# Optimization experiments

Hardware: AMD Instinct MI355X
Metric: run time of the kernel (lower is better)

Reference implementation:

```python
import jax, jax.numpy as jnp
import numpy as np

C = 256          # conv_channels
C1 = C // 2      # 128
C2 = C // 4      # 64
G = 1            # relation_glimpse


def setup_inputs() -> dict:
    key = jax.random.key(0)
    ks = jax.random.split(key, 20)
    bs, Nr, in_dim, q_dim = 4, 256, 2052, 1024
    d_in = in_dim + 4  # pos (first 4 coords) re-appended
    s = 0.02
    inp = {
        "Q": jax.random.normal(ks[0], (bs, q_dim), jnp.float32),
        "X": jax.random.normal(ks[1], (bs, Nr, in_dim), jnp.float32),
        "Wv": jax.random.normal(ks[2], (d_in, C), jnp.float32) * s,
        "bv": jnp.zeros((C,), jnp.float32),
        "Wq": jax.random.normal(ks[3], (q_dim, C), jnp.float32) * s,
        "bq": jnp.zeros((C,), jnp.float32),
        # branch 0 (r_conv01/02/03): 1x1 convs == per-position dense
        "W01": jax.random.normal(ks[4], (C, C1), jnp.float32) * s,
        "b01": jnp.zeros((C1,), jnp.float32),
        "W02": jax.random.normal(ks[5], (C1, C2), jnp.float32) * s,
        "b02": jnp.zeros((C2,), jnp.float32),
        "W03": jax.random.normal(ks[6], (C2, G), jnp.float32) * s,
        "b03": jnp.zeros((G,), jnp.float32),
        # branch 1 (r_conv1/2/3): dilation on 1x1 kernels is a no-op
        "W1": jax.random.normal(ks[7], (C, C1), jnp.float32) * s,
        "b1": jnp.zeros((C1,), jnp.float32),
        "W2": jax.random.normal(ks[8], (C1, C2), jnp.float32) * s,
        "b2": jnp.zeros((C2,), jnp.float32),
        "W3": jax.random.normal(ks[9], (C2, G), jnp.float32) * s,
        "b3": jnp.zeros((G,), jnp.float32),
    }
    return inp


def _mlp3(P, Wa, ba, Wb, bb, Wc, bc):
    # P: [bs, Nr, Nr, C]; three 1x1-conv layers, ReLU after each (incl. last).
    h = jax.nn.relu(jnp.einsum("bijc,ck->bijk", P, Wa) + ba)
    h = jax.nn.relu(jnp.einsum("bijc,ck->bijk", h, Wb) + bb)
    h = jax.nn.relu(jnp.einsum("bijc,ck->bijk", h, Wc) + bc)
    return h[..., 0]  # [bs, Nr, Nr] (relation_glimpse == 1)


def _attn_map(h):
    # symmetrize, then softmax over all Nr*Nr positions
    s = h + jnp.swapaxes(h, 1, 2)
    bs, Nr, _ = s.shape
    return jax.nn.softmax(s.reshape(bs, Nr * Nr), axis=-1).reshape(bs, Nr, Nr)


def reference(Q, X, Wv, bv, Wq, bq, W01, b01, W02, b02, W03, b03,
              W1, b1, W2, b2, W3, b3):
    X_ = X
    # append pos (first 4 coords) -> [bs, Nr, in_dim+4]
    Xcat = jnp.concatenate([X, X[:, :, :4]], axis=2)
    Xp = jnp.einsum("bnd,dc->bnc", Xcat, Wv) + bv
    Qp = Q @ Wq + bq
    Xp = Xp + Qp[:, None, :]                       # [bs, Nr, C]
    P = Xp[:, None, :, :] * Xp[:, :, None, :]      # [bs, Nr, Nr, C] pairwise product
    m0 = _attn_map(_mlp3(P, W01, b01, W02, b02, W03, b03))
    m1 = _attn_map(_mlp3(P, W1, b1, W2, b2, W3, b3))
    # weighted aggregation with original features; /(2*glimpse), then sum over Nr
    rel = jnp.einsum("bij,bjd->bid", m0 + m1, X_) / (2.0 * G)
    return rel.sum(axis=1)  # [bs, in_dim]
```

## Files before the change

kernel.cpp:

```cpp
#include <hip/hip_runtime.h>
#include <hip/hip_bf16.h>

typedef __attribute__((ext_vector_type(8)))  short short8;
typedef __attribute__((ext_vector_type(4)))  float f32x4;
typedef __attribute__((ext_vector_type(16))) float f32x16;

#define NR 256
#define CC 256

__device__ __forceinline__ unsigned short f2bf(float x) {
    union { float f; unsigned int u; } v; v.f = x;
    unsigned int r = v.u + 0x7FFFu + ((v.u >> 16) & 1u);
    return (unsigned short)(r >> 16);
}

__device__ __forceinline__ unsigned int pk2bf(float a, float b) {
    __hip_bfloat162 h = __float22bfloat162_rn(make_float2(a, b));
    union { __hip_bfloat162 h; unsigned int u; } cv; cv.h = h;
    return cv.u;
}

__global__ __launch_bounds__(256) void setup_kernel(
    const float* __restrict__ Q, const float* __restrict__ Wq, float* __restrict__ Qpp,
    const float* __restrict__ Wv, unsigned short* __restrict__ wvp,
    const float* __restrict__ W01, const float* __restrict__ W1,
    const float* __restrict__ W02, const float* __restrict__ W2,
    unsigned short* __restrict__ wpa, unsigned short* __restrict__ wpb)
{
    __shared__ float tile[32][260];
    __shared__ float qs[256];
    const int bx = blockIdx.x;
    const int tid = threadIdx.x;

    if (bx < 16) {
        int ksl = bx & 3, b = bx >> 2;
        qs[tid] = Q[b * 1024 + ksl * 256 + tid];
        __syncthreads();
        float acc = 0.f;
        #pragma unroll 4
        for (int d = 0; d < 256; ++d) acc += qs[d] * Wq[(size_t)(ksl * 256 + d) * 256 + tid];
        Qpp[(ksl * 4 + b) * 256 + tid] = acc;
    } else if (bx < 81) {
        int ks = bx - 16;
        for (int idx = tid; idx < 32 * 256; idx += 256) {
            int cr = idx >> 8, n = idx & 255;
            int c = ks * 32 + cr;
            tile[cr][n] = (c < 2056) ? Wv[(size_t)c * 256 + n] : 0.f;
        }
        __syncthreads();
        #pragma unroll
        for (int q = 0; q < 4; ++q) {
            int t2 = tid * 4 + q;
            int nt = t2 >> 6, l = t2 & 63;
            int gg = l >> 4, jj = l & 15;
            short8 s;
            #pragma unroll
            for (int e = 0; e < 8; ++e)
                s[e] = (short)f2bf(tile[gg * 8 + e][nt * 16 + jj]);
            *(short8*)&wvp[((size_t)(ks * 16 + nt) * 64 + l) * 8] = s;
        }
    } else {
        int t = (bx - 81) * 256 + tid;
        if (t < 65536) {
            int e = t & 7, l = (t >> 3) & 63, ks = (t >> 9) & 15, nt = (t >> 13) & 3, br = (t >> 15) & 1;
            int cc = ks * 16 + (l >> 5) * 8 + e;
            int n = nt * 32 + (l & 31);
            const float* W = br ? W1 : W01;
            wpa[t] = f2bf(W[cc * 128 + n]);
        } else {
            int t2 = t - 65536;
            int e = t2 & 7, l = (t2 >> 3) & 63, ks = (t2 >> 9) & 7, nt = (t2 >> 12) & 1, br = (t2 >> 13) & 1;
            int cc = ks * 16 + (l >> 5) * 8 + e;
            int n = nt * 32 + (l & 31);
            const float* W = br ? W2 : W02;
            wpb[t2] = f2bf(W[cc * 64 + n]);
        }
    }
}

__global__ __launch_bounds__(512) void xp_kernel(
    const float* __restrict__ X, const unsigned short* __restrict__ wvp,
    const float* __restrict__ bv, const float* __restrict__ bq,
    const float* __restrict__ Qpp, float* __restrict__ Xp)
{
    __shared__ f32x4 red[8][2][65];
    const int tid = threadIdx.x;
    const int w = tid >> 6;
    const int lane = tid & 63;
    const int g = lane >> 4, j16 = lane & 15;
    const int mt = blockIdx.x;
    const int bn = blockIdx.y;
    const int b  = blockIdx.z;

    const int i0 = mt * 16;
    const int n0 = bn * 32;
    const float* xrow = X + ((size_t)(b * NR) + (i0 + j16)) * 2052;

    f32x4 acc[2] = {};

    for (int ks = w; ks < 64; ks += 8) {
        const int c0 = ks * 32 + g * 8;
        float4 xa = *(const float4*)(xrow + c0);
        float4 xb = *(const float4*)(xrow + c0 + 4);
        union { short8 s; unsigned int u[4]; } af;
        af.u[0] = pk2bf(xa.x, xa.y);
        af.u[1] = pk2bf(xa.z, xa.w);
        af.u[2] = pk2bf(xb.x, xb.y);
        af.u[3] = pk2bf(xb.z, xb.w);
        #pragma unroll
        for (int nt = 0; nt < 2; ++nt) {
            short8 bf = ((const short8*)wvp)[(size_t)(ks * 16 + bn * 2 + nt) * 64 + lane];
            acc[nt] = __builtin_amdgcn_mfma_f32_16x16x32_bf16(af.s, bf, acc[nt], 0, 0, 0);
        }
    }
    if (w == 0) {
        float xv[8];
        #pragma unroll
        for (int e = 0; e < 8; ++e) {
            int q = g * 8 + e;
            int csrc = (q < 4) ? (2048 + q) : (q - 4);
            xv[e] = xrow[csrc];
        }
        union { short8 s; unsigned int u[4]; } af;
        af.u[0] = pk2bf(xv[0], xv[1]);
        af.u[1] = pk2bf(xv[2], xv[3]);
        af.u[2] = pk2bf(xv[4], xv[5]);
        af.u[3] = pk2bf(xv[6], xv[7]);
        #pragma unroll
        for (int nt = 0; nt < 2; ++nt) {
            short8 bf = ((const short8*)wvp)[(size_t)(64 * 16 + bn * 2 + nt) * 64 + lane];
            acc[nt] = __builtin_amdgcn_mfma_f32_16x16x32_bf16(af.s, bf, acc[nt], 0, 0, 0);
        }
    }
    #pragma unroll
    for (int nt = 0; nt < 2; ++nt) red[w][nt][lane] = acc[nt];
    __syncthreads();

    {
        int nt  = tid >> 8;
        int rem = tid & 255;
        int l   = rem & 63;
        int reg = (rem >> 6) & 3;
        float r = 0.f;
        #pragma unroll
        for (int ww = 0; ww < 8; ++ww) r += red[ww][nt][l][reg];
        int gg = l >> 4, jj = l & 15;
        int n = n0 + nt * 16 + jj;
        float base = bv[n] + bq[n] + Qpp[b * 256 + n] + Qpp[(4 + b) * 256 + n]
                   + Qpp[(8 + b) * 256 + n] + Qpp[(12 + b) * 256 + n];
        int row = i0 + gg * 4 + reg;
        Xp[((b * NR) + row) * CC + n] = r + base;
    }
}

__global__ __launch_bounds__(256, 2) void pairs_kernel(
    const float* __restrict__ Xp,
    const unsigned short* __restrict__ wpa,
    const unsigned short* __restrict__ wpb,
    const float* __restrict__ b01, const float* __restrict__ b02,
    const float* __restrict__ b03,
    const float* __restrict__ b1,  const float* __restrict__ b2,
    const float* __restrict__ b3,
    const float* __restrict__ W03, const float* __restrict__ W3,
    float* __restrict__ colpart, float* __restrict__ rowpart)
{
    __shared__ __align__(16) unsigned short lds_wa[16384];
    __shared__ __align__(16) float lds_si[1024];
    __shared__ __align__(16) float lds_bias1[128];
    __shared__ __align__(16) float lds_bias2[64];
    __shared__ __align__(16) float lds_w3[64];
    __shared__ float lds_c[4][33];

    const int tid = threadIdx.x;
    const int wave = tid >> 6;
    const int lane = tid & 63;
    const int hi = lane >> 5;
    const int j32 = lane & 31;

    int bx = blockIdx.x;
    int b = bx / 576;
    int r = bx - b * 576;
    int br = r / 288;
    int u = r - br * 288;
    int k = 0, off = 0;
    while (u >= off + 8 * (8 - k)) { off += 8 * (8 - k); ++k; }
    int rel = u - off, wdt = 8 - k;
    int it = k * 8 + rel / wdt;
    int jt = k + rel % wdt;

    const int i0 = it * 4;
    const int i = i0 + wave;
    const int j0 = jt * 32;
    const int blk = br * 4 + b;

    {
        int c4 = lane * 4;
        *(float4*)&lds_si[wave * 256 + c4] =
            *(const float4*)&Xp[((b * NR) + i) * CC + c4];
    }

    {
        const uint4* gsrc = (const uint4*)(wpa + (size_t)br * 32768);
        uint4* sdst = (uint4*)lds_wa;
        #pragma unroll
        for (int kk = 0; kk < 8; ++kk) sdst[kk * 256 + tid] = gsrc[kk * 256 + tid];
    }
    if (tid < 128) lds_bias1[tid] = br ? b1[tid] : b01[tid];
    else if (tid < 192) lds_bias2[tid - 128] = br ? b2[tid - 128] : b02[tid - 128];
    else lds_w3[tid - 192] = br ? W3[tid - 192] : W03[tid - 192];
    const float b3v = br ? b3[0] : b03[0];

    const float* xr = Xp + ((size_t)(b * NR) + (j0 + j32)) * CC;
    const float* si = lds_si + wave * 256;
    short8 bfr[16];
    #pragma unroll
    for (int ks = 0; ks < 16; ++ks) {
        const int c0 = ks * 16 + hi * 8;
        float4 xa = *(const float4*)(xr + c0);
        float4 xb = *(const float4*)(xr + c0 + 4);
        float4 sa = *(const float4*)(si + c0);
        float4 sb = *(const float4*)(si + c0 + 4);
        union { short8 s; unsigned int u[4]; } f;
        f.u[0] = pk2bf(xa.x * sa.x, xa.y * sa.y);
        f.u[1] = pk2bf(xa.z * sa.z, xa.w * sa.w);
        f.u[2] = pk2bf(xb.x * sb.x, xb.y * sb.y);
        f.u[3] = pk2bf(xb.z * sb.z, xb.w * sb.w);
        bfr[ks] = f.s;
    }

    __syncthreads();

    const short8* gwa = (const short8*)wpa + (size_t)br * 4096;
    const short8* wb  = (const short8*)wpb + (size_t)br * 1024;

    f32x16 acc2[2];
    #pragma unroll
    for (int nt = 0; nt < 2; ++nt) {
        #pragma unroll
        for (int q = 0; q < 4; ++q) {
            const float* bb = &lds_bias2[nt * 32 + q * 8 + hi * 4];
            acc2[nt][q * 4 + 0] = bb[0];
            acc2[nt][q * 4 + 1] = bb[1];
            acc2[nt][q * 4 + 2] = bb[2];
            acc2[nt][q * 4 + 3] = bb[3];
        }
    }

    #pragma unroll
    for (int t = 0; t < 4; ++t) {
        f32x16 acc1;
        #pragma unroll
        for (int q = 0; q < 4; ++q) {
            const float* bb = &lds_bias1[t * 32 + q * 8 + hi * 4];
            acc1[q * 4 + 0] = bb[0];
            acc1[q * 4 + 1] = bb[1];
            acc1[q * 4 + 2] = bb[2];
            acc1[q * 4 + 3] = bb[3];
        }
        #pragma unroll
        for (int ks = 0; ks < 16; ++ks) {
            short8 wf = (t < 2)
                ? ((const short8*)lds_wa)[(t * 16 + ks) * 64 + lane]
                : gwa[(t * 16 + ks) * 64 + lane];
            acc1 = __builtin_amdgcn_mfma_f32_32x32x16_bf16(wf, bfr[ks], acc1, 0, 0, 0);
        }
        #pragma unroll
        for (int s = 0; s < 2; ++s) {
            const int bse = s * 8;
            float rA0 = fmaxf(acc1[bse + 0], 0.f), rA1 = fmaxf(acc1[bse + 1], 0.f);
            float rA2 = fmaxf(acc1[bse + 2], 0.f), rA3 = fmaxf(acc1[bse + 3], 0.f);
            float rB0 = fmaxf(acc1[bse + 4], 0.f), rB1 = fmaxf(acc1[bse + 5], 0.f);
            float rB2 = fmaxf(acc1[bse + 6], 0.f), rB3 = fmaxf(acc1[bse + 7], 0.f);
            unsigned int uA0 = pk2bf(rA0, rA1), uA1 = pk2bf(rA2, rA3);
            unsigned int uB0 = pk2bf(rB0, rB1), uB1 = pk2bf(rB2, rB3);
            unsigned int pA0 = __shfl_xor(uA0, 32, 64), pA1 = __shfl_xor(uA1, 32, 64);
            unsigned int pB0 = __shfl_xor(uB0, 32, 64), pB1 = __shfl_xor(uB1, 32, 64);
            union { short8 s8; unsigned int u[4]; } B2;
            B2.u[0] = hi ? pB0 : uA0;
            B2.u[1] = hi ? pB1 : uA1;
            B2.u[2] = hi ? uB0 : pA0;
            B2.u[3] = hi ? uB1 : pA1;
            const int ks2 = 2 * t + s;
            acc2[0] = __builtin_amdgcn_mfma_f32_32x32x16_bf16(wb[ks2 * 64 + lane], B2.s8, acc2[0], 0, 0, 0);
            acc2[1] = __builtin_amdgcn_mfma_f32_32x32x16_bf16(wb[(8 + ks2) * 64 + lane], B2.s8, acc2[1], 0, 0, 0);
        }
    }

    float part = 0.f;
    #pragma unroll
    for (int nt = 0; nt < 2; ++nt) {
        #pragma unroll
        for (int q = 0; q < 4; ++q) {
            const float* wv = &lds_w3[nt * 32 + q * 8 + hi * 4];
            part += fmaxf(acc2[nt][q * 4 + 0], 0.f) * wv[0];
            part += fmaxf(acc2[nt][q * 4 + 1], 0.f) * wv[1];
            part += fmaxf(acc2[nt][q * 4 + 2], 0.f) * wv[2];
            part += fmaxf(acc2[nt][q * 4 + 3], 0.f) * wv[3];
        }
    }
    part += __shfl_xor(part, 32, 64);
    const float h3 = fmaxf(part + b3v, 0.f);
    const float E = __expf(2.f * h3);
    const int j = j0 + j32;
    const float Ec = (j >= i) ? E : 0.f;
    float Er = (j >  i) ? E : 0.f;

    Er += __shfl_xor(Er, 1, 64);
    Er += __shfl_xor(Er, 2, 64);
    Er += __shfl_xor(Er, 4, 64);
    Er += __shfl_xor(Er, 8, 64);
    Er += __shfl_xor(Er, 16, 64);
    Er += __shfl_xor(Er, 32, 64);
    if (lane == 0)
        rowpart[((size_t)blk * NR + i) * 8 + jt] = 0.5f * Er;

    if (!hi) lds_c[wave][j32] = Ec;
    __syncthreads();
    if (tid < 32) {
        float c = lds_c[0][tid] + lds_c[1][tid] + lds_c[2][tid] + lds_c[3][tid];
        const int cnt = 8 * jt + 8;
        colpart[(size_t)blk * 9216 + 128 * jt * (jt + 1) + tid * cnt + it] = c;
    }
}

__global__ __launch_bounds__(256) void colsoft_final_kernel(
    const float* __restrict__ colpart, const float* __restrict__ rowpart,
    float* __restrict__ wn)
{
    const int blk = blockIdx.x;
    const int j = threadIdx.x;
    const int jt = j >> 5, j32l = j & 31;
    const int cnt = 8 * jt + 8;
    float cs = 0.f;
    const float* cp = colpart + (size_t)blk * 9216 + 128 * jt * (jt + 1) + j32l * cnt;
    for (int it2 = 0; it2 < cnt; ++it2) cs += cp[it2];
    const float* rp = rowpart + ((size_t)blk * NR + j) * 8;
    for (int q = jt; q < 8; ++q) cs += rp[q];

    __shared__ float red[256];
    red[j] = cs; __syncthreads();
    for (int s = 128; s > 0; s >>= 1) {
        if (j < s) red[j] += red[j + s];
        __syncthreads();
    }
    wn[blk * 256 + j] = cs / red[0];
}

__global__ __launch_bounds__(256) void agg_part_kernel(
    const float* __restrict__ X, const float* __restrict__ wn,
    float* __restrict__ apart)
{
    const int dc = blockIdx.x, b = blockIdx.y, jc = blockIdx.z;
    const int d = dc * 256 + threadIdx.x;
    __shared__ float wc[32];
    if (threadIdx.x < 32) {
        int j = jc * 32 + threadIdx.x;
        wc[threadIdx.x] = 0.5f * (wn[b * 256 + j] + wn[(4 + b) * 256 + j]);
    }
    __syncthreads();
    if (d < 2052) {
        const float* xp = X + (size_t)b * NR * 2052 + (size_t)jc * 32 * 2052 + d;
        float a0 = 0.f, a1 = 0.f, a2 = 0.f, a3 = 0.f;
        for (int rr = 0; rr < 32; rr += 4) {
            a0 += wc[rr + 0] * xp[(size_t)(rr + 0) * 2052];
            a1 += wc[rr + 1] * xp[(size_t)(rr + 1) * 2052];
            a2 += wc[rr + 2] * xp[(size_t)(rr + 2) * 2052];
            a3 += wc[rr + 3] * xp[(size_t)(rr + 3) * 2052];
        }
        apart[(size_t)(jc * 4 + b) * 2304 + d] = (a0 + a1) + (a2 + a3);
    }
}

__global__ __launch_bounds__(256) void agg_final_kernel(
    const float* __restrict__ apart, float* __restrict__ out)
{
    const int dc = blockIdx.x, b = blockIdx.y;
    const int d = dc * 256 + threadIdx.x;
    if (d < 2052) {
        float s = 0.f;
        #pragma unroll
        for (int jc = 0; jc < 8; ++jc) s += apart[(size_t)(jc * 4 + b) * 2304 + d];
        out[b * 2052 + d] = s;
    }
}

extern "C" void kernel_launch(void* const* d_in, const int* in_sizes, int n_in,
                              void* d_out, int out_size, void* d_ws, size_t ws_size,
                              hipStream_t stream) {
    const float* Q   = (const float*)d_in[0];
    const float* X   = (const float*)d_in[1];
    const float* Wv  = (const float*)d_in[2];
    const float* bv  = (const float*)d_in[3];
    const float* Wq  = (const float*)d_in[4];
    const float* bq  = (const float*)d_in[5];
    const float* W01 = (const float*)d_in[6];
    const float* b01 = (const float*)d_in[7];
    const float* W02 = (const float*)d_in[8];
    const float* b02 = (const float*)d_in[9];
    const float* W03 = (const float*)d_in[10];
    const float* b03 = (const float*)d_in[11];
    const float* W1  = (const float*)d_in[12];
    const float* b1  = (const float*)d_in[13];
    const float* W2  = (const float*)d_in[14];
    const float* b2  = (const float*)d_in[15];
    const float* W3  = (const float*)d_in[16];
    const float* b3  = (const float*)d_in[17];

    char* ws = (char*)d_ws;
    float* Xp   = (float*)(ws + 0);
    float* Qpp  = (float*)(ws + 1048576);
    float* wn   = (float*)(ws + 1064960);
    unsigned short* wpa = (unsigned short*)(ws + 1073152);
    unsigned short* wpb = (unsigned short*)(ws + 1204224);
    float* colpart = (float*)(ws + 1236992);
    float* rowpart = (float*)(ws + 1531904);
    unsigned short* wvp = (unsigned short*)(ws + 1236992);
    float* apart = (float*)(ws + 0);
    float* out = (float*)d_out;

    setup_kernel<<<401, 256, 0, stream>>>(Q, Wq, Qpp, Wv, wvp,
                                          W01, W1, W02, W2, wpa, wpb);
    xp_kernel<<<dim3(16, 8, 4), 512, 0, stream>>>(X, wvp, bv, bq, Qpp, Xp);
    pairs_kernel<<<2304, 256, 0, stream>>>(Xp, wpa, wpb, b01, b02, b03,
                                           b1, b2, b3, W03, W3, colpart, rowpart);
    colsoft_final_kernel<<<8, 256, 0, stream>>>(colpart, rowpart, wn);
    agg_part_kernel<<<dim3(9, 4, 8), 256, 0, stream>>>(X, wn, apart);
    agg_final_kernel<<<dim3(9, 4), 256, 0, stream>>>(apart, out);
}
```

Baseline: 109.2 us.

## Enlarge pairs_kernel tiles to 8 rows and two column tiles with full LDS weights

```diff
diff --git a/kernel.cpp b/kernel.cpp
--- a/kernel.cpp
+++ b/kernel.cpp
@@ -153,7 +153,7 @@
     }
 }
 
-__global__ __launch_bounds__(256, 2) void pairs_kernel(
+__global__ __launch_bounds__(512, 1) void pairs_kernel(
     const float* __restrict__ Xp,
     const unsigned short* __restrict__ wpa,
     const unsigned short* __restrict__ wpb,
@@ -164,12 +164,13 @@
     const float* __restrict__ W03, const float* __restrict__ W3,
     float* __restrict__ colpart, float* __restrict__ rowpart)
 {
-    __shared__ __align__(16) unsigned short lds_wa[16384];
-    __shared__ __align__(16) float lds_si[1024];
+    __shared__ __align__(16) unsigned short lds_wa[32768];
+    __shared__ __align__(16) unsigned short lds_wb[8192];
+    __shared__ __align__(16) float lds_si[2048];
     __shared__ __align__(16) float lds_bias1[128];
     __shared__ __align__(16) float lds_bias2[64];
     __shared__ __align__(16) float lds_w3[64];
-    __shared__ float lds_c[4][33];
+    __shared__ float lds_c[8][33];
 
     const int tid = threadIdx.x;
     const int wave = tid >> 6;
@@ -178,148 +179,156 @@
     const int j32 = lane & 31;
 
     int bx = blockIdx.x;
-    int b = bx / 576;
-    int r = bx - b * 576;
-    int br = r / 288;
-    int u = r - br * 288;
+    int b = bx / 160;
+    int r = bx - b * 160;
+    int br = r / 80;
+    int u = r - br * 80;
     int k = 0, off = 0;
-    while (u >= off + 8 * (8 - k)) { off += 8 * (8 - k); ++k; }
-    int rel = u - off, wdt = 8 - k;
-    int it = k * 8 + rel / wdt;
-    int jt = k + rel % wdt;
-
-    const int i0 = it * 4;
-    const int i = i0 + wave;
-    const int j0 = jt * 32;
+    while (k < 7) {
+        int cnt = 4 * ((9 - k) / 2);
+        if (u < off + cnt) break;
+        off += cnt; ++k;
+    }
+    int rel = u - off;
+    int bpi = (9 - k) / 2;
+    int it8 = 4 * k + rel / bpi;
+    int jt_a = k + 2 * (rel % bpi);
+
+    const int i = it8 * 8 + wave;
     const int blk = br * 4 + b;
 
+    *(float4*)&lds_si[wave * 256 + lane * 4] =
+        *(const float4*)&Xp[((b * NR) + i) * CC + lane * 4];
+
     {
-        int c4 = lane * 4;
-        *(float4*)&lds_si[wave * 256 + c4] =
-            *(const float4*)&Xp[((b * NR) + i) * CC + c4];
-    }
-
-    {
-        const uint4* gsrc = (const uint4*)(wpa + (size_t)br * 32768);
-        uint4* sdst = (uint4*)lds_wa;
-        #pragma unroll
-        for (int kk = 0; kk < 8; ++kk) sdst[kk * 256 + tid] = gsrc[kk * 256 + tid];
-    }
-    if (tid < 128) lds_bias1[tid] = br ? b1[tid] : b01[tid];
-    else if (tid < 192) lds_bias2[tid - 128] = br ? b2[tid - 128] : b02[tid - 128];
-    else lds_w3[tid - 192] = br ? W3[tid - 192] : W03[tid - 192];
+        const uint4* g1 = (const uint4*)(wpa + (size_t)br * 32768);
+        uint4* s1 = (uint4*)lds_wa;
+        #pragma unroll
+        for (int kk = 0; kk < 8; ++kk) s1[kk * 512 + tid] = g1[kk * 512 + tid];
+        const uint4* g2 = (const uint4*)(wpb + (size_t)br * 8192);
+        uint4* s2 = (uint4*)lds_wb;
+        #pragma unroll
+        for (int kk = 0; kk < 2; ++kk) s2[kk * 512 + tid] = g2[kk * 512 + tid];
+        if (tid < 128) lds_bias1[tid] = br ? b1[tid] : b01[tid];
+        else if (tid < 192) lds_bias2[tid - 128] = br ? b2[tid - 128] : b02[tid - 128];
+        else if (tid < 256) lds_w3[tid - 192] = br ? W3[tid - 192] : W03[tid - 192];
+    }
+    __syncthreads();
     const float b3v = br ? b3[0] : b03[0];
-
-    const float* xr = Xp + ((size_t)(b * NR) + (j0 + j32)) * CC;
     const float* si = lds_si + wave * 256;
-    short8 bfr[16];
-    #pragma unroll
-    for (int ks = 0; ks < 16; ++ks) {
-        const int c0 = ks * 16 + hi * 8;
-        float4 xa = *(const float4*)(xr + c0);
-        float4 xb = *(const float4*)(xr + c0 + 4);
-        float4 sa = *(const float4*)(si + c0);
-        float4 sb = *(const float4*)(si + c0 + 4);
-        union { short8 s; unsigned int u[4]; } f;
-        f.u[0] = pk2bf(xa.x * sa.x, xa.y * sa.y);
-        f.u[1] = pk2bf(xa.z * sa.z, xa.w * sa.w);
-        f.u[2] = pk2bf(xb.x * sb.x, xb.y * sb.y);
-        f.u[3] = pk2bf(xb.z * sb.z, xb.w * sb.w);
-        bfr[ks] = f.s;
-    }
-
-    __syncthreads();
-
-    const short8* gwa = (const short8*)wpa + (size_t)br * 4096;
-    const short8* wb  = (const short8*)wpb + (size_t)br * 1024;
-
-    f32x16 acc2[2];
-    #pragma unroll
-    for (int nt = 0; nt < 2; ++nt) {
-        #pragma unroll
-        for (int q = 0; q < 4; ++q) {
-            const float* bb = &lds_bias2[nt * 32 + q * 8 + hi * 4];
-            acc2[nt][q * 4 + 0] = bb[0];
-            acc2[nt][q * 4 + 1] = bb[1];
-            acc2[nt][q * 4 + 2] = bb[2];
-            acc2[nt][q * 4 + 3] = bb[3];
-        }
-    }
-
-    #pragma unroll
-    for (int t = 0; t < 4; ++t) {
-        f32x16 acc1;
-        #pragma unroll
-        for (int q = 0; q < 4; ++q) {
-            const float* bb = &lds_bias1[t * 32 + q * 8 + hi * 4];
-            acc1[q * 4 + 0] = bb[0];
-            acc1[q * 4 + 1] = bb[1];
-            acc1[q * 4 + 2] = bb[2];
-            acc1[q * 4 + 3] = bb[3];
-        }
+
+    for (int pj = 0; pj < 2; ++pj) {
+        const int jt = jt_a + pj;
+        if (jt >= 8) break;
+        const int j0 = jt * 32;
+        const int j = j0 + j32;
+
+        const float* xr = Xp + ((size_t)(b * NR) + j) * CC;
+        short8 bfr[16];
         #pragma unroll
         for (int ks = 0; ks < 16; ++ks) {
-            short8 wf = (t < 2)
-                ? ((const short8*)lds_wa)[(t * 16 + ks) * 64 + lane]
-                : gwa[(t * 16 + ks) * 64 + lane];
-            acc1 = __builtin_amdgcn_mfma_f32_32x32x16_bf16(wf, bfr[ks], acc1, 0, 0, 0);
-        }
-        #pragma unroll
-        for (int s = 0; s < 2; ++s) {
-            const int bse = s * 8;
-            float rA0 = fmaxf(acc1[bse + 0], 0.f), rA1 = fmaxf(acc1[bse + 1], 0.f);
-            float rA2 = fmaxf(acc1[bse + 2], 0.f), rA3 = fmaxf(acc1[bse + 3], 0.f);
-            float rB0 = fmaxf(acc1[bse + 4], 0.f), rB1 = fmaxf(acc1[bse + 5], 0.f);
-            float rB2 = fmaxf(acc1[bse + 6], 0.f), rB3 = fmaxf(acc1[bse + 7], 0.f);
-            unsigned int uA0 = pk2bf(rA0, rA1), uA1 = pk2bf(rA2, rA3);
-            unsigned int uB0 = pk2bf(rB0, rB1), uB1 = pk2bf(rB2, rB3);
-            unsigned int pA0 = __shfl_xor(uA0, 32, 64), pA1 = __shfl_xor(uA1, 32, 64);
-            unsigned int pB0 = __shfl_xor(uB0, 32, 64), pB1 = __shfl_xor(uB1, 32, 64);
-            union { short8 s8; unsigned int u[4]; } B2;
-            B2.u[0] = hi ? pB0 : uA0;
-            B2.u[1] = hi ? pB1 : uA1;
-            B2.u[2] = hi ? uB0 : pA0;
-            B2.u[3] = hi ? uB1 : pA1;
-            const int ks2 = 2 * t + s;
-            acc2[0] = __builtin_amdgcn_mfma_f32_32x32x16_bf16(wb[ks2 * 64 + lane], B2.s8, acc2[0], 0, 0, 0);
-            acc2[1] = __builtin_amdgcn_mfma_f32_32x32x16_bf16(wb[(8 + ks2) * 64 + lane], B2.s8, acc2[1], 0, 0, 0);
-        }
-    }
-
-    float part = 0.f;
-    #pragma unroll
-    for (int nt = 0; nt < 2; ++nt) {
-        #pragma unroll
-        for (int q = 0; q < 4; ++q) {
-            const float* wv = &lds_w3[nt * 32 + q * 8 + hi * 4];
-            part += fmaxf(acc2[nt][q * 4 + 0], 0.f) * wv[0];
-            part += fmaxf(acc2[nt][q * 4 + 1], 0.f) * wv[1];
-            part += fmaxf(acc2[nt][q * 4 + 2], 0.f) * wv[2];
-            part += fmaxf(acc2[nt][q * 4 + 3], 0.f) * wv[3];
-        }
-    }
-    part += __shfl_xor(part, 32, 64);
-    const float h3 = fmaxf(part + b3v, 0.f);
-    const float E = __expf(2.f * h3);
-    const int j = j0 + j32;
-    const float Ec = (j >= i) ? E : 0.f;
-    float Er = (j >  i) ? E : 0.f;
-
-    Er += __shfl_xor(Er, 1, 64);
-    Er += __shfl_xor(Er, 2, 64);
-    Er += __shfl_xor(Er, 4, 64);
-    Er += __shfl_xor(Er, 8, 64);
-    Er += __shfl_xor(Er, 16, 64);
-    Er += __shfl_xor(Er, 32, 64);
-    if (lane == 0)
-        rowpart[((size_t)blk * NR + i) * 8 + jt] = 0.5f * Er;
-
-    if (!hi) lds_c[wave][j32] = Ec;
-    __syncthreads();
-    if (tid < 32) {
-        float c = lds_c[0][tid] + lds_c[1][tid] + lds_c[2][tid] + lds_c[3][tid];
-        const int cnt = 8 * jt + 8;
-        colpart[(size_t)blk * 9216 + 128 * jt * (jt + 1) + tid * cnt + it] = c;
+            const int c0 = ks * 16 + hi * 8;
+            float4 xa = *(const float4*)(xr + c0);
+            float4 xb = *(const float4*)(xr + c0 + 4);
+            float4 sa = *(const float4*)(si + c0);
+            float4 sb = *(const float4*)(si + c0 + 4);
+            union { short8 s; unsigned int uu[4]; } f;
+            f.uu[0] = pk2bf(xa.x * sa.x, xa.y * sa.y);
+            f.uu[1] = pk2bf(xa.z * sa.z, xa.w * sa.w);
+            f.uu[2] = pk2bf(xb.x * sb.x, xb.y * sb.y);
+            f.uu[3] = pk2bf(xb.z * sb.z, xb.w * sb.w);
+            bfr[ks] = f.s;
+        }
+
+        f32x16 acc2[2];
+        #pragma unroll
+        for (int nt = 0; nt < 2; ++nt) {
+            #pragma unroll
+            for (int q = 0; q < 4; ++q) {
+                const float* bb = &lds_bias2[nt * 32 + q * 8 + hi * 4];
+                acc2[nt][q * 4 + 0] = bb[0];
+                acc2[nt][q * 4 + 1] = bb[1];
+                acc2[nt][q * 4 + 2] = bb[2];
+                acc2[nt][q * 4 + 3] = bb[3];
+            }
+        }
+
+        #pragma unroll
+        for (int t = 0; t < 4; ++t) {
+            f32x16 acc1;
+            #pragma unroll
+            for (int q = 0; q < 4; ++q) {
+                const float* bb = &lds_bias1[t * 32 + q * 8 + hi * 4];
+                acc1[q * 4 + 0] = bb[0];
+                acc1[q * 4 + 1] = bb[1];
+                acc1[q * 4 + 2] = bb[2];
+                acc1[q * 4 + 3] = bb[3];
+            }
+            #pragma unroll
+            for (int ks = 0; ks < 16; ++ks) {
+                short8 wf = ((const short8*)lds_wa)[(t * 16 + ks) * 64 + lane];
+                acc1 = __builtin_amdgcn_mfma_f32_32x32x16_bf16(wf, bfr[ks], acc1, 0, 0, 0);
+            }
+            #pragma unroll
+            for (int s = 0; s < 2; ++s) {
+                const int bse = s * 8;
+                float rA0 = fmaxf(acc1[bse + 0], 0.f), rA1 = fmaxf(acc1[bse + 1], 0.f);
+                float rA2 = fmaxf(acc1[bse + 2], 0.f), rA3 = fmaxf(acc1[bse + 3], 0.f);
+                float rB0 = fmaxf(acc1[bse + 4], 0.f), rB1 = fmaxf(acc1[bse + 5], 0.f);
+                float rB2 = fmaxf(acc1[bse + 6], 0.f), rB3 = fmaxf(acc1[bse + 7], 0.f);
+                unsigned int uA0 = pk2bf(rA0, rA1), uA1 = pk2bf(rA2, rA3);
+                unsigned int uB0 = pk2bf(rB0, rB1), uB1 = pk2bf(rB2, rB3);
+                unsigned int pA0 = __shfl_xor(uA0, 32, 64), pA1 = __shfl_xor(uA1, 32, 64);
+                unsigned int pB0 = __shfl_xor(uB0, 32, 64), pB1 = __shfl_xor(uB1, 32, 64);
+                union { short8 s8; unsigned int uu[4]; } B2;
+                B2.uu[0] = hi ? pB0 : uA0;
+                B2.uu[1] = hi ? pB1 : uA1;
+                B2.uu[2] = hi ? uB0 : pA0;
+                B2.uu[3] = hi ? uB1 : pA1;
+                const int ks2 = 2 * t + s;
+                short8 w20 = ((const short8*)lds_wb)[ks2 * 64 + lane];
+                short8 w21 = ((const short8*)lds_wb)[(8 + ks2) * 64 + lane];
+                acc2[0] = __builtin_amdgcn_mfma_f32_32x32x16_bf16(w20, B2.s8, acc2[0], 0, 0, 0);
+                acc2[1] = __builtin_amdgcn_mfma_f32_32x32x16_bf16(w21, B2.s8, acc2[1], 0, 0, 0);
+            }
+        }
+
+        float part = 0.f;
+        #pragma unroll
+        for (int nt = 0; nt < 2; ++nt) {
+            #pragma unroll
+            for (int q = 0; q < 4; ++q) {
+                const float* wv = &lds_w3[nt * 32 + q * 8 + hi * 4];
+                part += fmaxf(acc2[nt][q * 4 + 0], 0.f) * wv[0];
+                part += fmaxf(acc2[nt][q * 4 + 1], 0.f) * wv[1];
+                part += fmaxf(acc2[nt][q * 4 + 2], 0.f) * wv[2];
+                part += fmaxf(acc2[nt][q * 4 + 3], 0.f) * wv[3];
+            }
+        }
+        part += __shfl_xor(part, 32, 64);
+        const float h3 = fmaxf(part + b3v, 0.f);
+        const float E = __expf(2.f * h3);
+        const float Ec = (j >= i) ? E : 0.f;
+        float Er = (j >  i) ? E : 0.f;
+
+        Er += __shfl_xor(Er, 1, 64);
+        Er += __shfl_xor(Er, 2, 64);
+        Er += __shfl_xor(Er, 4, 64);
+        Er += __shfl_xor(Er, 8, 64);
+        Er += __shfl_xor(Er, 16, 64);
+        Er += __shfl_xor(Er, 32, 64);
+        if (lane == 0)
+            rowpart[((size_t)blk * NR + i) * 8 + jt] = 0.5f * Er;
+
+        if (!hi) lds_c[wave][j32] = Ec;
+        __syncthreads();
+        if (tid < 32) {
+            float c = 0.f;
+            #pragma unroll
+            for (int w2 = 0; w2 < 8; ++w2) c += lds_c[w2][tid];
+            colpart[(size_t)blk * 4608 + 64 * jt * (jt + 1) + tid * (4 * jt + 4) + it8] = c;
+        }
+        __syncthreads();
     }
 }
 
@@ -330,9 +339,9 @@
     const int blk = blockIdx.x;
     const int j = threadIdx.x;
     const int jt = j >> 5, j32l = j & 31;
-    const int cnt = 8 * jt + 8;
+    const int cnt = 4 * jt + 4;
     float cs = 0.f;
-    const float* cp = colpart + (size_t)blk * 9216 + 128 * jt * (jt + 1) + j32l * cnt;
+    const float* cp = colpart + (size_t)blk * 4608 + 64 * jt * (jt + 1) + j32l * cnt;
     for (int it2 = 0; it2 < cnt; ++it2) cs += cp[it2];
     const float* rp = rowpart + ((size_t)blk * NR + j) * 8;
     for (int q = jt; q < 8; ++q) cs += rp[q];
@@ -413,7 +422,7 @@
     unsigned short* wpa = (unsigned short*)(ws + 1073152);
     unsigned short* wpb = (unsigned short*)(ws + 1204224);
     float* colpart = (float*)(ws + 1236992);
-    float* rowpart = (float*)(ws + 1531904);
+    float* rowpart = (float*)(ws + 1384448);
     unsigned short* wvp = (unsigned short*)(ws + 1236992);
     float* apart = (float*)(ws + 0);
     float* out = (float*)d_out;
@@ -421,8 +430,8 @@
     setup_kernel<<<401, 256, 0, stream>>>(Q, Wq, Qpp, Wv, wvp,
                                           W01, W1, W02, W2, wpa, wpb);
     xp_kernel<<<dim3(16, 8, 4), 512, 0, stream>>>(X, wvp, bv, bq, Qpp, Xp);
-    pairs_kernel<<<2304, 256, 0, stream>>>(Xp, wpa, wpb, b01, b02, b03,
-                                           b1, b2, b3, W03, W3, colpart, rowpart);
+    pairs_kernel<<<640, 512, 0, stream>>>(Xp, wpa, wpb, b01, b02, b03,
+                                          b1, b2, b3, W03, W3, colpart, rowpart);
     colsoft_final_kernel<<<8, 256, 0, stream>>>(colpart, rowpart, wn);
     agg_part_kernel<<<dim3(9, 4, 8), 256, 0, stream>>>(X, wn, apart);
     agg_final_kernel<<<dim3(9, 4), 256, 0, stream>>>(apart, out);
```

Result: slower. 112.1 us (+2.7%).
